# Optimization experiments

Hardware: AMD Instinct MI355X
Metric: run time of the kernel (lower is better)

The kernel has to match this reference:

```python
import jax, jax.numpy as jnp
import numpy as np

N_TX, N_ACC, N_MER = 100000, 50000, 5000
HID, HEADS, OUT_CH, LAYERS = 128, 4, 64, 3
HC = HID * HEADS  # 512, concat-heads width
SRC_T = ['tx', 'tx', 'tx', 'acc', 'acc', 'mer']
DST_T = ['acc', 'acc', 'mer', 'tx', 'tx', 'tx']


def setup_inputs():
    key = jax.random.key(0)
    ks = jax.random.split(key, 16)
    rn = lambda k, s: jax.random.normal(k, s, dtype=jnp.float32) * 0.05
    n_of = {'tx': N_TX, 'acc': N_ACC, 'mer': N_MER}
    E = N_TX  # one sender-acct / receiver-acct / merchant edge per transaction
    src = jnp.stack([jax.random.randint(jax.random.fold_in(ks[0], r), (E,), 0, n_of[SRC_T[r]]) for r in range(6)])
    dst = jnp.stack([jax.random.randint(jax.random.fold_in(ks[1], r), (E,), 0, n_of[DST_T[r]]) for r in range(6)])
    edges = jnp.stack([src, dst], axis=1).astype(jnp.int32)  # [6, 2, E] (rel, src/dst, edge)
    return dict(
        x_tx=rn(ks[2], (N_TX, 64)), x_acc=rn(ks[3], (N_ACC, 32)), x_mer=rn(ks[4], (N_MER, 32)),
        Wtx=rn(ks[5], (64, HID)), btx=jnp.zeros((HID,), jnp.float32),
        Wacc=rn(ks[6], (32, HID)), bacc=jnp.zeros((HID,), jnp.float32),
        Wmer=rn(ks[7], (32, HID)), bmer=jnp.zeros((HID,), jnp.float32),
        W0=rn(ks[8], (6, HID, HC)),            # layer-0 GAT linear per relation
        Wrest=rn(ks[9], (LAYERS - 1, 6, HC, HC)),  # layers 1..L-1
        att_s=rn(ks[10], (LAYERS, 6, HEADS, HID)),
        att_d=rn(ks[11], (LAYERS, 6, HEADS, HID)),
        att_b=jnp.zeros((LAYERS, 6, HC), jnp.float32),
        bn_g=jnp.ones((LAYERS, HC), jnp.float32), bn_b=jnp.zeros((LAYERS, HC), jnp.float32),
        Wh1=rn(ks[12], (HC, OUT_CH)), bh1=jnp.zeros((OUT_CH,), jnp.float32),
        Wh2=rn(ks[13], (OUT_CH, 1)), bh2=jnp.zeros((1,), jnp.float32),
        edges=edges)


def _gat_rel(x_src, x_dst, src, dst, W, a_s, a_d, b, n_dst):
    """PyG GATConv (shared lin, add_self_loops=False, concat heads), eval mode."""
    H, C = a_s.shape
    hs = (x_src @ W).reshape(-1, H, C)  # [Ns, H, C]
    hd = (x_dst @ W).reshape(-1, H, C)  # [Nd, H, C]
    e = jax.nn.leaky_relu((hs * a_s).sum(-1)[src] + (hd * a_d).sum(-1)[dst], 0.2)  # [E, H]
    m = jax.lax.stop_gradient(jax.ops.segment_max(e, dst, num_segments=n_dst))
    ex = jnp.exp(e - m[dst])
    denom = jax.ops.segment_sum(ex, dst, num_segments=n_dst)
    alpha = ex / (denom[dst] + 1e-16)  # segment softmax over in-edges of each dst
    out = jax.ops.segment_sum(alpha[:, :, None] * hs[src], dst, num_segments=n_dst)
    return out.reshape(n_dst, H * C) + b


def _forward(x_tx, x_acc, x_mer, Wtx, btx, Wacc, bacc, Wmer, bmer, W0, Wrest,
             att_s, att_d, att_b, bn_g, bn_b, Wh1, bh1, Wh2, bh2, edges):
    h = {'tx': jax.nn.relu(x_tx @ Wtx + btx),
         'acc': jax.nn.relu(x_acc @ Wacc + bacc),
         'mer': jax.nn.relu(x_mer @ Wmer + bmer)}
    n_of = {'tx': x_tx.shape[0], 'acc': x_acc.shape[0], 'mer': x_mer.shape[0]}
    for i in range(LAYERS):
        Wl = W0 if i == 0 else Wrest[i - 1]
        new = {k: jnp.zeros((n_of[k], HC), x_tx.dtype) for k in n_of}  # HeteroConv aggr='sum'
        for r in range(6):
            o = _gat_rel(h[SRC_T[r]], h[DST_T[r]], edges[r, 0], edges[r, 1],
                         Wl[r], att_s[i, r], att_d[i, r], att_b[i, r], n_of[DST_T[r]])
            new[DST_T[r]] = new[DST_T[r]] + o
        t = new['tx']  # BatchNorm1d (batch statistics) on transaction nodes only
        mu = t.mean(0)
        var = t.var(0)
        new['tx'] = (t - mu) / jnp.sqrt(var + 1e-5) * bn_g[i] + bn_b[i]
        new = {k: jax.nn.relu(v) for k, v in new.items()}
        if i > 0:  # residual from second layer on
            new = {k: new[k] + h[k] for k in new}
        h = new
    hidden = jax.nn.relu(h['tx'] @ Wh1 + bh1)
    return (hidden @ Wh2 + bh2).squeeze(-1)  # [N_tx] logits


def reference(x_tx, x_acc, x_mer, Wtx, btx, Wacc, bacc, Wmer, bmer, W0, Wrest,
              att_s, att_d, att_b, bn_g, bn_b, Wh1, bh1, Wh2, bh2, edges):
    return _forward(x_tx, x_acc, x_mer, Wtx, btx, Wacc, bacc, Wmer, bmer, W0, Wrest,
                    att_s, att_d, att_b, bn_g, bn_b, Wh1, bh1, Wh2, bh2, edges)
```

## Files before the change

kernel.cpp:

```cpp
#include <hip/hip_runtime.h>
#include <math.h>


typedef unsigned short BF16;
typedef short short8 __attribute__((ext_vector_type(8)));
typedef float f32x4 __attribute__((ext_vector_type(4)));
typedef __bf16 bf16x8 __attribute__((ext_vector_type(8)));

static __device__ __forceinline__ float lrelu(float x){ return x > 0.f ? x : 0.2f*x; }

__device__ __forceinline__ float ldE(const float* p, long i){ return p[i]; }
__device__ __forceinline__ float ldE(const BF16* p, long i){
  return __uint_as_float((unsigned)p[i] << 16);
}
__device__ __forceinline__ void stE(float* p, long i, float v){ p[i] = v; }
__device__ __forceinline__ void stE(BF16* p, long i, float v){
  unsigned u = __float_as_uint(v);
  p[i] = (BF16)((u + 0x7FFFu + ((u >> 16) & 1u)) >> 16);
}
__device__ __forceinline__ BF16 f2bf(float v){
  unsigned u = __float_as_uint(v);
  return (BF16)((u + 0x7FFFu + ((u >> 16) & 1u)) >> 16);
}
__device__ __forceinline__ float bf2f(short s){
  return __uint_as_float((unsigned)(unsigned short)s << 16);
}
__device__ __forceinline__ float4 ld4E(const float* p, long i){ return *(const float4*)(p + i); }
__device__ __forceinline__ float4 ld4E(const BF16* p, long i){
  ushort4 s = *(const ushort4*)(p + i);
  return make_float4(__uint_as_float((unsigned)s.x<<16), __uint_as_float((unsigned)s.y<<16),
                     __uint_as_float((unsigned)s.z<<16), __uint_as_float((unsigned)s.w<<16));
}

__global__ void k_zero(int* __restrict__ p, long n){
  long i = (long)blockIdx.x*blockDim.x + threadIdx.x;
  if (i < n) p[i] = 0;
}
__global__ void k_fill_f32(float* __restrict__ p, long n, float v){
  long i = (long)blockIdx.x*blockDim.x + threadIdx.x;
  if (i < n) p[i] = v;
}

__global__ __launch_bounds__(256) void k_wt(const float* __restrict__ in, BF16* __restrict__ out,
                                            int K, int N)
{
  in  += (long)blockIdx.z*K*N;
  out += (long)blockIdx.z*N*K;
  __shared__ float t[32][33];
  int kb = blockIdx.y*32, nb = blockIdx.x*32;
  int tx = threadIdx.x & 31, ty8 = threadIdx.x >> 5;
  for (int j = ty8; j < 32; j += 8){
    int k = kb + j, n = nb + tx;
    t[j][tx] = (k < K && n < N) ? in[(long)k*N + n] : 0.f;
  }
  __syncthreads();
  for (int j = ty8; j < 32; j += 8){
    int n = nb + j, k = kb + tx;
    if (n < N && k < K) out[(long)n*K + k] = f2bf(t[tx][j]);
  }
}

__global__ __launch_bounds__(256) void k_foldAll(
    const float* __restrict__ Wbase, long wstride,
    const float* __restrict__ atts, const float* __restrict__ attd,
    float* __restrict__ F, int Din)
{
  int w = (blockIdx.x*256 + threadIdx.x) >> 6;
  int lane = threadIdx.x & 63;
  int total = 48*Din;
  if (w >= total) return;
  int k = w % Din;
  int rem = w / Din;
  int h = rem & 3, sd = (rem >> 2) & 1, r = rem >> 3;
  const float* wr = Wbase + (long)r*wstride + (long)k*512 + h*128;
  const float* ar = (sd ? attd : atts) + r*512 + h*128;
  float p = wr[lane]*ar[lane] + wr[lane+64]*ar[lane+64];
  #pragma unroll
  for (int off = 32; off; off >>= 1) p += __shfl_down(p, off, 64);
  if (lane == 0) F[(long)((r*2+sd)*4 + h)*Din + k] = p;
}

template<int BN, int WM, int WN, int FM, int FN, typename TC>
__global__ __launch_bounds__(256) void k_mfma(
    const BF16* __restrict__ A, const BF16* __restrict__ Bt, TC* __restrict__ C,
    int M, int K, int c0, int ldc, int lda, const float* __restrict__ bias,
    int doRelu, int accum, long aZst, long cZst, int c0Zst, const BF16* __restrict__ Bt1)
{
  constexpr int BM = 128;
  constexpr int LSTR = 72;
  __shared__ __attribute__((aligned(16))) short Als[BM][LSTR];
  __shared__ __attribute__((aligned(16))) short Bls[BN][LSTR];
  const int z = blockIdx.z;
  A += (long)z*aZst;
  C += (long)z*cZst;
  c0 += z*c0Zst;
  if (z >= 1 && Bt1) Bt = Bt1;
  const int bn0 = blockIdx.x * BN;
  const int bm = blockIdx.y*BM;
  const int tid = threadIdx.x;
  const int wave = tid >> 6, lane = tid & 63;
  const int wr = wave / WN, wc = wave % WN;
  const int lrow = lane & 15, kg = lane >> 4;
  f32x4 acc[FM][FN] = {};
  for (int k0 = 0; k0 < K; k0 += 64){
    #pragma unroll
    for (int t = 0; t < 4; ++t){
      int idx = tid + t*256;
      int row = idx >> 3, kc = (idx & 7) << 3;
      int gr = bm + row;
      short8 v = {};
      if (gr < M) v = *(const short8*)(A + (long)gr*lda + k0 + kc);
      *(short8*)&Als[row][kc] = v;
    }
    #pragma unroll
    for (int t = 0; t < BN/32; ++t){
      int idx = tid + t*256;
      int row = idx >> 3, kc = (idx & 7) << 3;
      *(short8*)&Bls[row][kc] = *(const short8*)(Bt + (long)(c0+bn0+row)*K + k0 + kc);
    }
    __syncthreads();
    #pragma unroll
    for (int kk = 0; kk < 2; ++kk){
      short8 af[FM], bq[FN];
      #pragma unroll
      for (int m = 0; m < FM; ++m)
        af[m] = *(const short8*)&Als[wr*FM*16 + m*16 + lrow][kk*32 + kg*8];
      #pragma unroll
      for (int n = 0; n < FN; ++n)
        bq[n] = *(const short8*)&Bls[wc*FN*16 + n*16 + lrow][kk*32 + kg*8];
      #pragma unroll
      for (int m = 0; m < FM; ++m)
        #pragma unroll
        for (int n = 0; n < FN; ++n)
          acc[m][n] = __builtin_amdgcn_mfma_f32_16x16x32_bf16(
              __builtin_bit_cast(bf16x8, af[m]), __builtin_bit_cast(bf16x8, bq[n]),
              acc[m][n], 0, 0, 0);
    }
    __syncthreads();
  }
  #pragma unroll
  for (int m = 0; m < FM; ++m){
    #pragma unroll
    for (int n = 0; n < FN; ++n){
      #pragma unroll
      for (int j = 0; j < 4; ++j){
        int row = bm + wr*FM*16 + m*16 + kg*4 + j;
        if (row >= M) continue;
        int col = wc*FN*16 + n*16 + lrow;
        float v = acc[m][n][j];
        if (bias) v += bias[bn0 + col];
        if (doRelu) v = fmaxf(v, 0.f);
        long idx = (long)row*ldc + bn0 + col;
        if (accum) v += ldE(C, idx);
        stE(C, idx, v);
      }
    }
  }
}

template<typename TA, typename TC>
__global__ __launch_bounds__(256) void k_gemm(
    const TA* __restrict__ A, const float* __restrict__ B, TC* __restrict__ C,
    int M, int N, int K, int ldb, const float* __restrict__ bias, int doRelu)
{
  __shared__ float As[16][64];
  __shared__ float Bs[16][64];
  const int bm = blockIdx.y*64, bn = blockIdx.x*64;
  const int tid = threadIdx.x;
  const int ty = tid >> 4, tx = tid & 15;
  const int ar = tid >> 2;
  const int ac = (tid & 3) << 2;
  const int br = tid >> 4;
  const int bc = (tid & 15) << 2;
  float acc[4][4] = {};
  for (int k0 = 0; k0 < K; k0 += 16){
    int row = bm + ar;
    float4 av = make_float4(0.f,0.f,0.f,0.f);
    if (row < M) av = ld4E(A, (long)row*K + k0 + ac);
    As[ac+0][ar]=av.x; As[ac+1][ar]=av.y; As[ac+2][ar]=av.z; As[ac+3][ar]=av.w;
    float4 bv = make_float4(0.f,0.f,0.f,0.f);
    if (bn + bc + 3 < N) bv = *(const float4*)(B + (long)(k0+br)*ldb + bn + bc);
    *(float4*)&Bs[br][bc] = bv;
    __syncthreads();
    #pragma unroll
    for (int kk = 0; kk < 16; ++kk){
      float a[4], b[4];
      #pragma unroll
      for (int x = 0; x < 4; ++x){ a[x]=As[kk][ty*4+x]; b[x]=Bs[kk][tx*4+x]; }
      #pragma unroll
      for (int y = 0; y < 4; ++y)
        #pragma unroll
        for (int x = 0; x < 4; ++x) acc[y][x] += a[y]*b[x];
    }
    __syncthreads();
  }
  #pragma unroll
  for (int y = 0; y < 4; ++y){
    int row = bm + ty*4 + y;
    if (row >= M) continue;
    #pragma unroll
    for (int x = 0; x < 4; ++x){
      int col = bn + tx*4 + x;
      if (col >= N) continue;
      float v = acc[y][x];
      if (bias) v += bias[col];
      if (doRelu) v = fmaxf(v, 0.f);
      stE(C, (long)row*N + col, v);
    }
  }
}

template<int R>
__global__ __launch_bounds__(256) void k_scoreM(
    const BF16* __restrict__ X, const float* __restrict__ Ftab, long fstride,
    float* __restrict__ out, long ostride, int N, int Din)
{
  int wave = threadIdx.x >> 6, lane = threadIdx.x & 63;
  int node0 = blockIdx.x*16 + wave*4;
  if (node0 >= N) return;
  int base = lane*8;
  bool act = base < Din;
  float x[4][8];
  #pragma unroll
  for (int t = 0; t < 4; ++t){
    int node = node0 + t;
    if (act && node < N){
      short8 v = *(const short8*)(X + (long)node*Din + base);
      #pragma unroll
      for (int j = 0; j < 8; ++j) x[t][j] = bf2f(v[j]);
    } else {
      #pragma unroll
      for (int j = 0; j < 8; ++j) x[t][j] = 0.f;
    }
  }
  #pragma unroll
  for (int r = 0; r < R; ++r){
    const float* F = Ftab + (long)r*fstride;
    float p[4][4] = {};
    #pragma unroll
    for (int h = 0; h < 4; ++h){
      float f[8];
      if (act){
        float4 fa = *(const float4*)(F + h*Din + base);
        float4 fb = *(const float4*)(F + h*Din + base + 4);
        f[0]=fa.x; f[1]=fa.y; f[2]=fa.z; f[3]=fa.w;
        f[4]=fb.x; f[5]=fb.y; f[6]=fb.z; f[7]=fb.w;
      } else {
        #pragma unroll
        for (int j = 0; j < 8; ++j) f[j] = 0.f;
      }
      #pragma unroll
      for (int t = 0; t < 4; ++t)
        #pragma unroll
        for (int j = 0; j < 8; ++j) p[t][h] += x[t][j]*f[j];
    }
    #pragma unroll
    for (int t = 0; t < 4; ++t)
      #pragma unroll
      for (int h = 0; h < 4; ++h)
        #pragma unroll
        for (int off = 32; off; off >>= 1)
          p[t][h] += __shfl_down(p[t][h], off, 64);
    if (lane == 0){
      #pragma unroll
      for (int t = 0; t < 4; ++t){
        int node = node0 + t;
        if (node < N){
          #pragma unroll
          for (int h = 0; h < 4; ++h)
            out[(long)r*ostride + (long)node*4 + h] = p[t][h];
        }
      }
    }
  }
}

__global__ void k_hist(const int* __restrict__ dst, int* __restrict__ counts, int E, int nd){
  int e = blockIdx.x*blockDim.x + threadIdx.x;
  if (e >= E) return;
  int d = dst[e];
  if ((unsigned)d < (unsigned)nd) atomicAdd(&counts[d], 1);
}
__global__ void k_scan1(const int* __restrict__ counts, int* __restrict__ indptr,
                        int* __restrict__ bsums, int n)
{
  __shared__ int sm[256];
  int i = blockIdx.x*256 + threadIdx.x;
  int v = (i < n) ? counts[i] : 0;
  sm[threadIdx.x] = v; __syncthreads();
  for (int off = 1; off < 256; off <<= 1){
    int t = (threadIdx.x >= off) ? sm[threadIdx.x - off] : 0;
    __syncthreads();
    sm[threadIdx.x] += t;
    __syncthreads();
  }
  if (i < n) indptr[i+1] = sm[threadIdx.x];
  if (threadIdx.x == 255) bsums[blockIdx.x] = sm[255];
  if (blockIdx.x == 0 && threadIdx.x == 0) indptr[0] = 0;
}
__global__ void k_scan2(int* __restrict__ bsums, int nb){
  __shared__ int sm[1024];
  int t = threadIdx.x;
  int v = (t < nb) ? bsums[t] : 0;
  sm[t] = v; __syncthreads();
  for (int off = 1; off < 1024; off <<= 1){
    int x = (t >= off) ? sm[t - off] : 0;
    __syncthreads();
    sm[t] += x;
    __syncthreads();
  }
  if (t < nb) bsums[t] = sm[t];
}
__global__ void k_scan3(int* __restrict__ indptr, const int* __restrict__ bsums, int n){
  if (blockIdx.x == 0) return;
  int i = blockIdx.x*256 + threadIdx.x;
  int add = bsums[blockIdx.x - 1];
  if (i < n) indptr[i+1] += add;
}
__global__ void k_scatter(const int* __restrict__ src, const int* __restrict__ dst,
                          const int* __restrict__ indptr, int* __restrict__ cursor,
                          int* __restrict__ esrc, int E, int nd, int ns)
{
  int e = blockIdx.x*blockDim.x + threadIdx.x;
  if (e >= E) return;
  int d = dst[e];
  if ((unsigned)d >= (unsigned)nd) return;
  int s = src[e];
  if ((unsigned)s >= (unsigned)ns) s = 0;
  int pos = indptr[d] + atomicAdd(&cursor[d], 1);
  if (pos >= 0 && pos < E) esrc[pos] = s;
}

struct AlphaArgs {
  const float* ss[3]; const float* sd[3];
  const int* ip[3]; const int* es[3];
  float* al[3]; int nd[3]; int ns[3];
};
__global__ __launch_bounds__(256) void k_alpha3b(AlphaArgs a, int E){
  int r = blockIdx.y;
  int wid = (blockIdx.x*blockDim.x + threadIdx.x) >> 6;
  int lane = threadIdx.x & 63;
  if (wid >= a.nd[r]) return;
  const int* indptr = a.ip[r];
  const int* esrc = a.es[r];
  const float* ss = a.ss[r];
  int ns = a.ns[r];
  int e0 = indptr[wid], e1 = indptr[wid+1];
  e0 = max(0, min(e0, E)); e1 = max(e0, min(e1, E));
  if (e0 >= e1) return;
  int h = lane >> 4, g = lane & 15;
  float sdl = a.sd[r][(long)wid*4 + h];
  float* alpha = a.al[r];
  float m = -INFINITY;
  for (int e = e0 + g; e < e1; e += 16){
    int s = esrc[e]; if ((unsigned)s >= (unsigned)ns) s = 0;
    m = fmaxf(m, lrelu(ss[(long)s*4 + h] + sdl));
  }
  #pragma unroll
  for (int o = 1; o < 16; o <<= 1) m = fmaxf(m, __shfl_xor(m, o, 16));
  float den = 0.f;
  for (int e = e0 + g; e < e1; e += 16){
    int s = esrc[e]; if ((unsigned)s >= (unsigned)ns) s = 0;
    den += __expf(lrelu(ss[(long)s*4 + h] + sdl) - m);
  }
  #pragma unroll
  for (int o = 1; o < 16; o <<= 1) den += __shfl_xor(den, o, 16);
  float inv = 1.f/(den + 1e-16f);
  for (int e = e0 + g; e < e1; e += 16){
    int s = esrc[e]; if ((unsigned)s >= (unsigned)ns) s = 0;
    alpha[(long)e*4 + h] = __expf(lrelu(ss[(long)s*4 + h] + sdl) - m) * inv;
  }
}

template<int NJ>
__global__ __launch_bounds__(256) void k_gather4(
    const BF16* __restrict__ A, const float* __restrict__ alpha,
    const int* __restrict__ indptr, const int* __restrict__ esrc,
    BF16* __restrict__ G, int n_dst, int Din, int E, int ns)
{
  int wid = (blockIdx.x*blockDim.x + threadIdx.x) >> 6;
  int lane = threadIdx.x & 63;
  if (wid >= n_dst) return;
  int e0 = indptr[wid], e1 = indptr[wid+1];
  e0 = max(0, min(e0, E)); e1 = max(e0, min(e1, E));
  float acc[4][NJ];
  #pragma unroll
  for (int h = 0; h < 4; ++h)
    #pragma unroll
    for (int j = 0; j < NJ; ++j) acc[h][j] = 0.f;
  for (int e = e0; e < e1; ++e){
    int s = esrc[e]; if ((unsigned)s >= (unsigned)ns) s = 0;
    float a0 = alpha[(long)e*4 + 0], a1 = alpha[(long)e*4 + 1];
    float a2 = alpha[(long)e*4 + 2], a3 = alpha[(long)e*4 + 3];
    const BF16* ar = A + (long)s*Din;
    if (NJ == 8){
      short8 v = *(const short8*)(ar + lane*8);
      #pragma unroll
      for (int j = 0; j < NJ; ++j){
        float x = bf2f(v[j]);
        acc[0][j] += a0*x; acc[1][j] += a1*x; acc[2][j] += a2*x; acc[3][j] += a3*x;
      }
    } else {
      ushort2 v = *(const ushort2*)(ar + lane*2);
      float x0 = bf2f((short)v.x), x1 = bf2f((short)v.y);
      acc[0][0] += a0*x0; acc[1][0] += a1*x0; acc[2][0] += a2*x0; acc[3][0] += a3*x0;
      acc[0][1] += a0*x1; acc[1][1] += a1*x1; acc[2][1] += a2*x1; acc[3][1] += a3*x1;
    }
  }
  #pragma unroll
  for (int h = 0; h < 4; ++h){
    if (NJ == 8){
      short8 g;
      #pragma unroll
      for (int j = 0; j < NJ; ++j) g[j] = (short)f2bf(acc[h][j]);
      *(short8*)(G + ((long)wid*4 + h)*Din + lane*8) = g;
    } else {
      ushort2 g;
      g.x = f2bf(acc[h][0]); g.y = f2bf(acc[h][1]);
      *(ushort2*)(G + ((long)wid*4 + h)*Din + lane*2) = g;
    }
  }
}

template<int NJ>
__device__ __forceinline__ void agg_body(
    const BF16* __restrict__ Zt, const float* __restrict__ alpha,
    const int* __restrict__ indptr, const int* __restrict__ esrc,
    float* acc, int wid, int lane, int TW, int head0, int E, int ns)
{
  int e0 = indptr[wid], e1 = indptr[wid+1];
  e0 = max(0, min(e0, E)); e1 = max(e0, min(e1, E));
  for (int e = e0; e < e1; ++e){
    int s = esrc[e]; if ((unsigned)s >= (unsigned)ns) s = 0;
    float aA = alpha[(long)e*4 + head0];
    const BF16* zr = Zt + (long)s*TW;
    if (NJ == 2){
      ushort2 z = *(const ushort2*)(zr + lane*2);
      acc[0] += aA * bf2f((short)z.x);
      acc[1] += aA * bf2f((short)z.y);
    } else {
      acc[0] += aA * ldE(zr, lane);
    }
  }
}

template<int NJ>
__global__ __launch_bounds__(256) void k_agg2(
    const BF16* __restrict__ Z0, const BF16* __restrict__ Z1,
    const float* __restrict__ a0, const float* __restrict__ a1,
    const int* __restrict__ ip0, const int* __restrict__ ip1,
    const int* __restrict__ es0, const int* __restrict__ es1,
    BF16* __restrict__ out, int ldc, int c0w, int TW, int head0,
    int n_dst, int E, int ns0, int ns1)
{
  int wid = (blockIdx.x*blockDim.x + threadIdx.x) >> 6;
  int lane = threadIdx.x & 63;
  if (wid >= n_dst) return;
  float acc[NJ];
  #pragma unroll
  for (int j = 0; j < NJ; ++j) acc[j] = 0.f;
  agg_body<NJ>(Z0, a0, ip0, es0, acc, wid, lane, TW, head0, E, ns0);
  agg_body<NJ>(Z1, a1, ip1, es1, acc, wid, lane, TW, head0, E, ns1);
  if (NJ == 2){
    ushort2 g; g.x = f2bf(acc[0]); g.y = f2bf(acc[1]);
    *(ushort2*)(out + (long)wid*ldc + c0w + lane*2) = g;
  } else {
    stE(out, (long)wid*ldc + c0w + lane, acc[0]);
  }
}

template<int NJ>
__global__ __launch_bounds__(256) void k_agg3(
    const BF16* __restrict__ Z0, const BF16* __restrict__ Z1, const BF16* __restrict__ Z2,
    const float* __restrict__ a0, const float* __restrict__ a1, const float* __restrict__ a2,
    const int* __restrict__ ip0, const int* __restrict__ ip1, const int* __restrict__ ip2,
    const int* __restrict__ es0, const int* __restrict__ es1, const int* __restrict__ es2,
    BF16* __restrict__ out, int ldc, int TW, int head0,
    int n_dst, int E, int ns0, int ns1, int ns2)
{
  int wid = (blockIdx.x*blockDim.x + threadIdx.x) >> 6;
  int lane = threadIdx.x & 63;
  if (wid >= n_dst) return;
  float acc[NJ];
  #pragma unroll
  for (int j = 0; j < NJ; ++j) acc[j] = 0.f;
  agg_body<NJ>(Z0, a0, ip0, es0, acc, wid, lane, TW, head0, E, ns0);
  agg_body<NJ>(Z1, a1, ip1, es1, acc, wid, lane, TW, head0, E, ns1);
  agg_body<NJ>(Z2, a2, ip2, es2, acc, wid, lane, TW, head0, E, ns2);
  if (NJ == 2){
    ushort2 g; g.x = f2bf(acc[0]); g.y = f2bf(acc[1]);
    *(ushort2*)(out + (long)wid*ldc + lane*2) = g;
  } else {
    stE(out, (long)wid*ldc + lane, acc[0]);
  }
}

__global__ void k_bnp(const BF16* __restrict__ nw, float* __restrict__ bnp,
                      int N, int TW, int P)
{
  int col  = threadIdx.x & (TW - 1);
  int slot = threadIdx.x / TW;
  int rpb  = 256 / TW;
  int p    = blockIdx.x*rpb + slot;
  float s = 0.f, s2 = 0.f;
  for (long r = p; r < N; r += P){
    float v = ldE(nw, r*TW + col);
    s += v; s2 += v*v;
  }
  bnp[(long)p*2*TW + col]      = s;
  bnp[(long)p*2*TW + TW + col] = s2;
}
__global__ void k_bnf(const float* __restrict__ bnp, float* __restrict__ bns,
                      int P, int TW)
{
  int c = blockIdx.x*256 + threadIdx.x;
  if (c >= 2*TW) return;
  float s = 0.f;
  for (int p = 0; p < P; ++p) s += bnp[(long)p*2*TW + c];
  bns[c] = s;
}
__global__ void k_bn_apply(const BF16* __restrict__ nw, const float* __restrict__ bns,
                           const float* __restrict__ g, const float* __restrict__ b,
                           BF16* __restrict__ A, int N, int TW, int c0, int res)
{
  long total8 = (long)N*TW/8;
  for (long i8 = (long)blockIdx.x*blockDim.x + threadIdx.x; i8 < total8;
       i8 += (long)gridDim.x*blockDim.x){
    long i = i8*8;
    int col = (int)(i % TW);
    long r  = i / TW;
    short8 nv = *(const short8*)(nw + i);
    long ai = r*512 + c0 + col;
    short8 av;
    if (res) av = *(const short8*)(A + ai);
    short8 ov;
    #pragma unroll
    for (int k = 0; k < 8; ++k){
      int gc = c0 + col + k;
      float mu  = bns[col+k] / (float)N;
      float var = bns[TW + col + k] / (float)N - mu*mu;
      float sc = g[gc] * rsqrtf(var + 1e-5f);
      float sh = b[gc] - mu*sc;
      float v = fmaxf(bf2f(nv[k])*sc + sh, 0.f);
      if (res) v += bf2f(av[k]);
      ov[k] = (short)f2bf(v);
    }
    *(short8*)(A + ai) = ov;
  }
}

__global__ void k_update(const BF16* __restrict__ B, const float* __restrict__ ab1,
                         const float* __restrict__ ab2, BF16* __restrict__ A,
                         long n512, int res)
{
  long n8 = n512/8;
  for (long i8 = (long)blockIdx.x*blockDim.x + threadIdx.x; i8 < n8;
       i8 += (long)gridDim.x*blockDim.x){
    long i = i8*8;
    int c = (int)(i & 511);
    short8 bv = *(const short8*)(B + i);
    short8 av;
    if (res) av = *(const short8*)(A + i);
    short8 ov;
    #pragma unroll
    for (int k = 0; k < 8; ++k){
      float v = bf2f(bv[k]) + ab1[c+k] + (ab2 ? ab2[c+k] : 0.f);
      v = fmaxf(v, 0.f);
      if (res) v += bf2f(av[k]);
      ov[k] = (short)f2bf(v);
    }
    *(short8*)(A + i) = ov;
  }
}

__global__ void k_logits(const BF16* __restrict__ Hid, const float* __restrict__ Wh2,
                         const float* __restrict__ bh2, float* __restrict__ out, int N)
{
  int node = (blockIdx.x*blockDim.x + threadIdx.x) >> 6;
  int lane = threadIdx.x & 63;
  if (node >= N) return;
  float v = ldE(Hid, (long)node*64 + lane) * Wh2[lane];
  #pragma unroll
  for (int off = 32; off; off >>= 1) v += __shfl_down(v, off, 64);
  if (lane == 0) out[node] = v + bh2[0];
}

struct Arena {
  BF16 *A[3];
  BF16 *Bst[3];
  BF16 *Zt;
  BF16 *blkB;
  BF16 *hidden;
  float *scoreS, *scoreD;
  float *alpha;
  float *Fbuf;
  float *bnp, *bns;
  int *counts, *bsums;
  int *indptr[6], *esrc[6];
  BF16 *Wt0[6], *WtL[2][6], *Wh1t;
  size_t total;
};

extern "C" void kernel_launch(void* const* d_in, const int* in_sizes, int n_in,
                              void* d_out, int out_size, void* d_ws, size_t ws_size,
                              hipStream_t stream)
{
  const float* x_tx  = (const float*)d_in[0];
  const float* x_acc = (const float*)d_in[1];
  const float* x_mer = (const float*)d_in[2];
  const float* Wtx = (const float*)d_in[3];  const float* btx  = (const float*)d_in[4];
  const float* Wacc= (const float*)d_in[5];  const float* bacc = (const float*)d_in[6];
  const float* Wmer= (const float*)d_in[7];  const float* bmer = (const float*)d_in[8];
  const float* W0   = (const float*)d_in[9];
  const float* Wrest= (const float*)d_in[10];
  const float* att_s= (const float*)d_in[11];
  const float* att_d= (const float*)d_in[12];
  const float* att_b= (const float*)d_in[13];
  const float* bn_g = (const float*)d_in[14];
  const float* bn_b = (const float*)d_in[15];
  const float* Wh1  = (const float*)d_in[16]; const float* bh1 = (const float*)d_in[17];
  const float* Wh2  = (const float*)d_in[18]; const float* bh2 = (const float*)d_in[19];
  const int*   edges= (const int*)d_in[20];

  const int E    = in_sizes[20] / 12;
  const int nTx  = in_sizes[0] / 64;
  const int nAcc = in_sizes[1] / 32;
  const int nMer = in_sizes[2] / 32;
  const int nOf[3]   = {nTx, nAcc, nMer};
  const int SRC_T[6] = {0,0,0,1,1,2};
  const int DST_T[6] = {1,1,2,0,0,0};
  const int maxN = max(nTx, max(nAcc, nMer));
  (void)n_in;

  auto layout = [&](int TW)->Arena{
    Arena P{};
    size_t off = 0;
    auto a = [&](size_t bytes)->char*{
      char* p = (char*)d_ws + off;
      off += (bytes + 255) & ~(size_t)255;
      return p;
    };
    auto al = [](size_t b){ return (b + 255) & ~(size_t)255; };
    P.A[0]   = (BF16*)a((size_t)nTx *512*2);
    P.A[1]   = (BF16*)a((size_t)nAcc*512*2);
    P.A[2]   = (BF16*)a((size_t)nMer*512*2);
    P.Bst[1] = (BF16*)a((size_t)nAcc*512*2);
    P.Bst[2] = (BF16*)a((size_t)nMer*512*2);
    size_t zrowsA = (size_t)maxN > (size_t)2*nAcc + nMer ? (size_t)maxN : (size_t)2*nAcc + nMer;
    size_t blkA = al(zrowsA*TW*2);
    size_t blkBsz = al((size_t)nTx*TW*2);
    size_t gB = al((size_t)nMer*4*512*2);
    if (gB > blkBsz) blkBsz = gB;
    size_t scoreB = al((size_t)3*maxN*4*4)*2;
    size_t hidB = al((size_t)nTx*64*2);
    size_t scr = blkA + blkBsz;
    if (scr < scoreB) scr = scoreB;
    if (scr < hidB)   scr = hidB;
    char* scrBase = a(scr);
    P.Zt     = (BF16*)scrBase;
    P.blkB   = (BF16*)(scrBase + blkA);
    P.scoreS = (float*)scrBase;
    P.scoreD = (float*)(scrBase + al((size_t)3*maxN*4*4));
    P.hidden = (BF16*)scrBase;
    P.alpha  = (float*)a((size_t)3*E*4*4);
    P.Fbuf   = (float*)a((size_t)6*8*512*4);
    P.bnp    = (float*)a(262144);
    P.bns    = (float*)a(4096);
    P.counts = (int*)a((size_t)maxN*4);
    P.bsums  = (int*)a(4096);
    for (int r = 0; r < 6; ++r){
      P.indptr[r] = (int*)a((size_t)(nOf[DST_T[r]]+1)*4);
      P.esrc[r]   = (int*)a((size_t)E*4);
    }
    for (int r = 0; r < 6; ++r) P.Wt0[r] = (BF16*)a((size_t)512*128*2);
    for (int l = 0; l < 2; ++l)
      for (int r = 0; r < 6; ++r) P.WtL[l][r] = (BF16*)a((size_t)512*512*2);
    P.Wh1t = (BF16*)a((size_t)64*512*2);
    P.total = off;
    return P;
  };

  int TW = 0;
  Arena P{};
  for (int cand : {128, 64}){
    P = layout(cand);
    if (P.total <= ws_size){ TW = cand; break; }
  }
  if (TW == 0){
    float sentinel = 10000.0f + (float)(ws_size >> 20);
    k_fill_f32<<<dim3((out_size+255)/256), dim3(256), 0, stream>>>((float*)d_out, (long)out_size, sentinel);
    return;
  }
  const int nTiles = 512 / TW;
  const int NJv = TW/64;
  const int rpb = 256 / TW, PBX = 64, Pp = PBX * rpb;
  dim3 b256(256);

  k_wt<<<dim3(16,4,6),  b256, 0, stream>>>(W0,    P.Wt0[0],    128, 512);
  k_wt<<<dim3(16,16,12),b256, 0, stream>>>(Wrest, P.WtL[0][0], 512, 512);
  k_wt<<<dim3(2,16,1),  b256, 0, stream>>>(Wh1,   P.Wh1t,      512, 64);

  auto mfma_gemm = [&](const BF16* A, const BF16* Bt, BF16* Cp, int M, int K, int c0, int ldc){
    if (TW >= 128)
      k_mfma<128,2,2,4,4,BF16><<<dim3(TW/128,(M+127)/128,1),b256,0,stream>>>(
          A, Bt, Cp, M, K, c0, ldc, K, (const float*)nullptr, 0, 0, 0L, 0L, 0, (const BF16*)nullptr);
    else
      k_mfma<64,4,1,2,4,BF16><<<dim3(1,(M+127)/128,1),b256,0,stream>>>(
          A, Bt, Cp, M, K, c0, ldc, K, (const float*)nullptr, 0, 0, 0L, 0L, 0, (const BF16*)nullptr);
  };
  auto mfma_pair = [&](const BF16* A, const BF16* Bt0, const BF16* Bt1p, BF16* Cp, long cZst,
                       int M, int K, int c0){
    if (TW >= 128)
      k_mfma<128,2,2,4,4,BF16><<<dim3(TW/128,(M+127)/128,2),b256,0,stream>>>(
          A, Bt0, Cp, M, K, c0, TW, K, (const float*)nullptr, 0, 0, 0L, cZst, 0, Bt1p);
    else {
      mfma_gemm(A, Bt0, Cp, M, K, c0, TW);
      mfma_gemm(A, Bt1p, Cp + cZst, M, K, c0, TW);
    }
  };

  for (int r = 0; r < 6; ++r){
    int nd = nOf[DST_T[r]], ns = nOf[SRC_T[r]];
    const int* srcP = edges + (size_t)r*2*E;
    const int* dstP = srcP + E;
    int nb = (nd + 255)/256;
    k_zero   <<<dim3(nb),          b256, 0, stream>>>(P.counts, (long)nd);
    k_hist   <<<dim3((E+255)/256), b256, 0, stream>>>(dstP, P.counts, E, nd);
    k_scan1  <<<dim3(nb),          b256, 0, stream>>>(P.counts, P.indptr[r], P.bsums, nd);
    k_scan2  <<<dim3(1),           dim3(1024),0, stream>>>(P.bsums, nb);
    k_scan3  <<<dim3(nb),          b256, 0, stream>>>(P.indptr[r], P.bsums, nd);
    k_zero   <<<dim3(nb),          b256, 0, stream>>>(P.counts, (long)nd);
    k_scatter<<<dim3((E+255)/256), b256, 0, stream>>>(srcP, dstP, P.indptr[r], P.counts, P.esrc[r], E, nd, ns);
  }

  k_gemm<float,BF16><<<dim3(2,(nTx +63)/64), b256, 0, stream>>>(x_tx,  Wtx,  P.A[0], nTx,  128, 64, 128, btx,  1);
  k_gemm<float,BF16><<<dim3(2,(nAcc+63)/64), b256, 0, stream>>>(x_acc, Wacc, P.A[1], nAcc, 128, 32, 128, bacc, 1);
  k_gemm<float,BF16><<<dim3(2,(nMer+63)/64), b256, 0, stream>>>(x_mer, Wmer, P.A[2], nMer, 128, 32, 128, bmer, 1);

  const long mS = (long)maxN*4;
  for (int i = 0; i < 3; ++i){
    const int Din = (i == 0) ? 128 : 512;
    const int res = (i > 0) ? 1 : 0;
    const long fstr = 8L*Din;
    const float* WbaseL = (i == 0) ? W0 : (Wrest + (size_t)(i-1)*6*512*512);
    const long wstride = (i == 0) ? 128L*512 : 512L*512;
    auto Wtof = [&](int r)->const BF16*{ return (i == 0) ? P.Wt0[r] : P.WtL[i-1][r]; };

    k_foldAll<<<dim3(48*Din/4), b256, 0, stream>>>(WbaseL, wstride,
        att_s + (size_t)i*6*512, att_d + (size_t)i*6*512, P.Fbuf, Din);

    k_scoreM<3><<<dim3((nTx+15)/16), b256, 0, stream>>>(P.A[0], P.Fbuf,           fstr, P.scoreS, mS, nTx, Din);
    k_scoreM<2><<<dim3((nAcc+15)/16), b256, 0, stream>>>(P.A[1], P.Fbuf + 4*Din,  fstr, P.scoreD, mS, nAcc, Din);
    k_scoreM<1><<<dim3((nMer+15)/16), b256, 0, stream>>>(P.A[2], P.Fbuf + 20*Din, fstr, P.scoreD + 2*mS, 0, nMer, Din);
    {
      AlphaArgs aa{};
      int ndMax = 0;
      for (int r = 0; r < 3; ++r){
        aa.ss[r] = P.scoreS + r*mS; aa.sd[r] = P.scoreD + r*mS;
        aa.ip[r] = P.indptr[r]; aa.es[r] = P.esrc[r];
        aa.al[r] = P.alpha + (size_t)r*E*4;
        aa.nd[r] = nOf[DST_T[r]]; aa.ns[r] = nTx;
        if (aa.nd[r] > ndMax) ndMax = aa.nd[r];
      }
      k_alpha3b<<<dim3((ndMax+3)/4,3), b256, 0, stream>>>(aa, E);
    }
    {
      BF16* Gm = P.blkB;
      if (Din == 512)
        k_gather4<8><<<dim3((nMer+3)/4), b256, 0, stream>>>(P.A[0], P.alpha + (size_t)2*E*4,
            P.indptr[2], P.esrc[2], Gm, nMer, Din, E, nTx);
      else
        k_gather4<2><<<dim3((nMer+3)/4), b256, 0, stream>>>(P.A[0], P.alpha + (size_t)2*E*4,
            P.indptr[2], P.esrc[2], Gm, nMer, Din, E, nTx);
      k_mfma<128,2,2,4,4,BF16><<<dim3(1,(nMer+127)/128,4), b256, 0, stream>>>(
          Gm, Wtof(2), P.Bst[2], nMer, Din, 0, 512, 4*Din,
          (const float*)nullptr, 0, 0, (long)Din, 128L, 128, (const BF16*)nullptr);
    }
    {
      BF16* Zr0 = P.Zt;
      BF16* Zr1 = P.blkB;
      long zst = (long)(Zr1 - Zr0);
      for (int t = 0; t < nTiles; ++t){
        int c0 = t*TW;
        mfma_pair(P.A[0], Wtof(0), Wtof(1), Zr0, zst, nTx, Din, c0);
        dim3 ga((nAcc+3)/4);
        if (NJv == 2)
          k_agg2<2><<<ga,b256,0,stream>>>(Zr0, Zr1, P.alpha, P.alpha + (size_t)E*4,
              P.indptr[0], P.indptr[1], P.esrc[0], P.esrc[1],
              P.Bst[1], 512, c0, TW, c0>>7, nAcc, E, nTx, nTx);
        else
          k_agg2<1><<<ga,b256,0,stream>>>(Zr0, Zr1, P.alpha, P.alpha + (size_t)E*4,
              P.indptr[0], P.indptr[1], P.esrc[0], P.esrc[1],
              P.Bst[1], 512, c0, TW, c0>>7, nAcc, E, nTx, nTx);
      }
    }

    k_scoreM<2><<<dim3((nAcc+15)/16), b256, 0, stream>>>(P.A[1], P.Fbuf + 24*Din, fstr, P.scoreS, mS, nAcc, Din);
    k_scoreM<1><<<dim3((nMer+15)/16), b256, 0, stream>>>(P.A[2], P.Fbuf + 40*Din, fstr, P.scoreS + 2*mS, 0, nMer, Din);
    k_scoreM<3><<<dim3((nTx+15)/16), b256, 0, stream>>>(P.A[0], P.Fbuf + 28*Din, fstr, P.scoreD, mS, nTx, Din);
    {
      AlphaArgs aa{};
      for (int q = 0; q < 3; ++q){
        int r = 3 + q;
        aa.ss[q] = P.scoreS + q*mS; aa.sd[q] = P.scoreD + q*mS;
        aa.ip[q] = P.indptr[r]; aa.es[q] = P.esrc[r];
        aa.al[q] = P.alpha + (size_t)q*E*4;
        aa.nd[q] = nTx; aa.ns[q] = nOf[SRC_T[r]];
      }
      k_alpha3b<<<dim3((nTx+3)/4,3), b256, 0, stream>>>(aa, E);
    }
    BF16* Z3 = P.Zt;
    BF16* Z4 = P.Zt + (size_t)nAcc*TW;
    BF16* Z5 = P.Zt + (size_t)2*nAcc*TW;
    BF16* nw = P.blkB;
    for (int t = 0; t < nTiles; ++t){
      int c0 = t*TW;
      mfma_pair(P.A[1], Wtof(3), Wtof(4), Z3, (long)nAcc*TW, nAcc, Din, c0);
      mfma_gemm(P.A[2], Wtof(5), Z5, nMer, Din, c0, TW);
      dim3 ga((nTx+3)/4);
      if (NJv == 2)
        k_agg3<2><<<ga,b256,0,stream>>>(Z3,Z4,Z5, P.alpha, P.alpha+(size_t)E*4, P.alpha+(size_t)2*E*4,
            P.indptr[3],P.indptr[4],P.indptr[5], P.esrc[3],P.esrc[4],P.esrc[5],
            nw, TW, TW, c0>>7, nTx, E, nAcc, nAcc, nMer);
      else
        k_agg3<1><<<ga,b256,0,stream>>>(Z3,Z4,Z5, P.alpha, P.alpha+(size_t)E*4, P.alpha+(size_t)2*E*4,
            P.indptr[3],P.indptr[4],P.indptr[5], P.esrc[3],P.esrc[4],P.esrc[5],
            nw, TW, TW, c0>>7, nTx, E, nAcc, nAcc, nMer);
      k_bnp<<<dim3(PBX), b256, 0, stream>>>(nw, P.bnp, nTx, TW, Pp);
      k_bnf<<<dim3((2*TW+255)/256), b256, 0, stream>>>(P.bnp, P.bns, Pp, TW);
      k_bn_apply<<<dim3(2048), b256, 0, stream>>>(nw, P.bns,
          bn_g + (size_t)i*512, bn_b + (size_t)i*512, P.A[0], nTx, TW, c0, res);
    }
    const float* ab0 = att_b + ((size_t)(i*6 + 0))*512;
    const float* ab1 = att_b + ((size_t)(i*6 + 1))*512;
    const float* ab2 = att_b + ((size_t)(i*6 + 2))*512;
    k_update<<<dim3(1024), b256, 0, stream>>>(P.Bst[1], ab0, ab1, P.A[1], (long)nAcc*512, res);
    k_update<<<dim3(128),  b256, 0, stream>>>(P.Bst[2], ab2, (const float*)nullptr, P.A[2], (long)nMer*512, res);
  }

  k_mfma<64,4,1,2,4,BF16><<<dim3(1,(nTx+127)/128,1), b256, 0, stream>>>(
      P.A[0], P.Wh1t, P.hidden, nTx, 512, 0, 64, 512, bh1, 1, 0,
      0L, 0L, 0, (const BF16*)nullptr);
  k_logits<<<dim3((nTx+3)/4), b256, 0, stream>>>(P.hidden, Wh2, bh2, (float*)d_out, nTx);
}
```

Before: 10.12 ms.

## Load GEMM tiles directly to LDS and vectorize BatchNorm partial sums

The MFMA GEMM now stages A and B tiles with global_load_lds (direct global-to-LDS DMA) instead of loading into registers and storing to LDS. The LDS layout drops its padding to the dense 64-wide rows that this instruction requires, and out-of-range rows are clamped to a valid row rather than zero-filled. The BatchNorm partial-sum kernel reads 8 bf16 values per thread with more partial slots, which needs a larger partial buffer. Removing the padding may bring LDS bank conflicts back on the fragment reads.

```diff
diff --git a/kernel.cpp b/kernel.cpp
--- a/kernel.cpp
+++ b/kernel.cpp
@@ -30,6 +30,12 @@
   ushort4 s = *(const ushort4*)(p + i);
   return make_float4(__uint_as_float((unsigned)s.x<<16), __uint_as_float((unsigned)s.y<<16),
                      __uint_as_float((unsigned)s.z<<16), __uint_as_float((unsigned)s.w<<16));
+}
+
+__device__ __forceinline__ void gl_lds16(const BF16* g, short* l){
+  __builtin_amdgcn_global_load_lds(
+      (const __attribute__((address_space(1))) void*)g,
+      (__attribute__((address_space(3))) void*)l, 16, 0, 0);
 }
 
 __global__ void k_zero(int* __restrict__ p, long n){
@@ -87,9 +93,8 @@
     int doRelu, int accum, long aZst, long cZst, int c0Zst, const BF16* __restrict__ Bt1)
 {
   constexpr int BM = 128;
-  constexpr int LSTR = 72;
-  __shared__ __attribute__((aligned(16))) short Als[BM][LSTR];
-  __shared__ __attribute__((aligned(16))) short Bls[BN][LSTR];
+  __shared__ __attribute__((aligned(16))) short AlsL[BM*64];
+  __shared__ __attribute__((aligned(16))) short BlsL[BN*64];
   const int z = blockIdx.z;
   A += (long)z*aZst;
   C += (long)z*cZst;
@@ -101,22 +106,22 @@
   const int wave = tid >> 6, lane = tid & 63;
   const int wr = wave / WN, wc = wave % WN;
   const int lrow = lane & 15, kg = lane >> 4;
+  const int lr8 = lane >> 3, lc8 = (lane & 7) << 3;
   f32x4 acc[FM][FN] = {};
   for (int k0 = 0; k0 < K; k0 += 64){
     #pragma unroll
-    for (int t = 0; t < 4; ++t){
-      int idx = tid + t*256;
-      int row = idx >> 3, kc = (idx & 7) << 3;
+    for (int t = 0; t < BM/32; ++t){
+      int rb = (wave*(BM/32) + t)*8;
+      int row = rb + lr8;
       int gr = bm + row;
-      short8 v = {};
-      if (gr < M) v = *(const short8*)(A + (long)gr*lda + k0 + kc);
-      *(short8*)&Als[row][kc] = v;
+      if (gr >= M) gr = bm;
+      gl_lds16(A + (long)gr*lda + k0 + lc8, &AlsL[rb*64]);
     }
     #pragma unroll
     for (int t = 0; t < BN/32; ++t){
-      int idx = tid + t*256;
-      int row = idx >> 3, kc = (idx & 7) << 3;
-      *(short8*)&Bls[row][kc] = *(const short8*)(Bt + (long)(c0+bn0+row)*K + k0 + kc);
+      int rb = (wave*(BN/32) + t)*8;
+      int row = rb + lr8;
+      gl_lds16(Bt + (long)(c0+bn0+row)*K + k0 + lc8, &BlsL[rb*64]);
     }
     __syncthreads();
     #pragma unroll
@@ -124,10 +129,10 @@
       short8 af[FM], bq[FN];
       #pragma unroll
       for (int m = 0; m < FM; ++m)
-        af[m] = *(const short8*)&Als[wr*FM*16 + m*16 + lrow][kk*32 + kg*8];
+        af[m] = *(const short8*)&AlsL[(wr*FM*16 + m*16 + lrow)*64 + kk*32 + kg*8];
       #pragma unroll
       for (int n = 0; n < FN; ++n)
-        bq[n] = *(const short8*)&Bls[wc*FN*16 + n*16 + lrow][kk*32 + kg*8];
+        bq[n] = *(const short8*)&BlsL[(wc*FN*16 + n*16 + lrow)*64 + kk*32 + kg*8];
       #pragma unroll
       for (int m = 0; m < FM; ++m)
         #pragma unroll
@@ -498,17 +503,25 @@
 __global__ void k_bnp(const BF16* __restrict__ nw, float* __restrict__ bnp,
                       int N, int TW, int P)
 {
-  int col  = threadIdx.x & (TW - 1);
-  int slot = threadIdx.x / TW;
-  int rpb  = 256 / TW;
+  int cpr  = TW/8;
+  int col  = (threadIdx.x % cpr)*8;
+  int slot = threadIdx.x / cpr;
+  int rpb  = 256 / cpr;
   int p    = blockIdx.x*rpb + slot;
-  float s = 0.f, s2 = 0.f;
+  float s[8] = {}, s2[8] = {};
   for (long r = p; r < N; r += P){
-    float v = ldE(nw, r*TW + col);
-    s += v; s2 += v*v;
-  }
-  bnp[(long)p*2*TW + col]      = s;
-  bnp[(long)p*2*TW + TW + col] = s2;
+    short8 v = *(const short8*)(nw + r*TW + col);
+    #pragma unroll
+    for (int k = 0; k < 8; ++k){
+      float x = bf2f(v[k]);
+      s[k] += x; s2[k] += x*x;
+    }
+  }
+  #pragma unroll
+  for (int k = 0; k < 8; ++k){
+    bnp[(long)p*2*TW + col + k]      = s[k];
+    bnp[(long)p*2*TW + TW + col + k] = s2[k];
+  }
 }
 __global__ void k_bnf(const float* __restrict__ bnp, float* __restrict__ bns,
                       int P, int TW)
@@ -664,7 +677,7 @@
     P.hidden = (BF16*)scrBase;
     P.alpha  = (float*)a((size_t)3*E*4*4);
     P.Fbuf   = (float*)a((size_t)6*8*512*4);
-    P.bnp    = (float*)a(262144);
+    P.bnp    = (float*)a(1048576);
     P.bns    = (float*)a(4096);
     P.counts = (int*)a((size_t)maxN*4);
     P.bsums  = (int*)a(4096);
@@ -693,7 +706,7 @@
   }
   const int nTiles = 512 / TW;
   const int NJv = TW/64;
-  const int rpb = 256 / TW, PBX = 64, Pp = PBX * rpb;
+  const int PBX = 64, Pp = PBX * (256/(TW/8));
   dim3 b256(256);
 
   k_wt<<<dim3(16,4,6),  b256, 0, stream>>>(W0,    P.Wt0[0],    128, 512);
```

Result: slower. 17.81 ms (+76.1%).

## Fuse paired relation GEMMs into one 128x256 MFMA kernel sharing A tiles

Applied to the files above, without the earlier changes.

Adds a 512-thread MFMA kernel, k_mfma2, that computes both projections of the paired GEMM in a single block. It stages one A tile in LDS and a combined 256-row B tile built from Bt0 and Bt1, then writes the two 128-column halves to separate outputs. Before, a z=2 grid launched two blocks per row tile, and each loaded the same A tile. The change is meant to halve A global traffic and cut the block count, at the cost of more LDS per block, a larger accumulator footprint and possibly lower occupancy. The new launch uses a grid x-dimension of 1, so it assumes a tile width of 128.

```diff
diff --git a/kernel.cpp b/kernel.cpp
--- a/kernel.cpp
+++ b/kernel.cpp
@@ -153,6 +153,75 @@
         long idx = (long)row*ldc + bn0 + col;
         if (accum) v += ldE(C, idx);
         stE(C, idx, v);
+      }
+    }
+  }
+}
+
+__global__ __launch_bounds__(512) void k_mfma2(
+    const BF16* __restrict__ A, const BF16* __restrict__ Bt0, const BF16* __restrict__ Bt1,
+    BF16* __restrict__ C0, BF16* __restrict__ C1,
+    int M, int K, int c0, int ldc, int lda)
+{
+  constexpr int BM = 128, BN = 256, LSTR = 72;
+  __shared__ __attribute__((aligned(16))) short Als[BM][LSTR];
+  __shared__ __attribute__((aligned(16))) short Bls[BN][LSTR];
+  const int bm = blockIdx.y*BM;
+  const int tid = threadIdx.x;
+  const int wave = tid >> 6, lane = tid & 63;
+  const int wr = wave >> 2, wc = wave & 3;
+  const int lrow = lane & 15, kg = lane >> 4;
+  f32x4 acc[4][4] = {};
+  for (int k0 = 0; k0 < K; k0 += 64){
+    #pragma unroll
+    for (int t = 0; t < 2; ++t){
+      int idx = tid + t*512;
+      int row = idx >> 3, kc = (idx & 7) << 3;
+      int gr = bm + row;
+      short8 v = {};
+      if (gr < M) v = *(const short8*)(A + (long)gr*lda + k0 + kc);
+      *(short8*)&Als[row][kc] = v;
+    }
+    #pragma unroll
+    for (int t = 0; t < 4; ++t){
+      int idx = tid + t*512;
+      int row = idx >> 3, kc = (idx & 7) << 3;
+      const BF16* src = (row < 128) ? (Bt0 + (long)(c0 + row)*K)
+                                    : (Bt1 + (long)(c0 + row - 128)*K);
+      *(short8*)&Bls[row][kc] = *(const short8*)(src + k0 + kc);
+    }
+    __syncthreads();
+    #pragma unroll
+    for (int kk = 0; kk < 2; ++kk){
+      short8 af[4], bq[4];
+      #pragma unroll
+      for (int m = 0; m < 4; ++m)
+        af[m] = *(const short8*)&Als[wr*64 + m*16 + lrow][kk*32 + kg*8];
+      #pragma unroll
+      for (int n = 0; n < 4; ++n)
+        bq[n] = *(const short8*)&Bls[wc*64 + n*16 + lrow][kk*32 + kg*8];
+      #pragma unroll
+      for (int m = 0; m < 4; ++m)
+        #pragma unroll
+        for (int n = 0; n < 4; ++n)
+          acc[m][n] = __builtin_amdgcn_mfma_f32_16x16x32_bf16(
+              __builtin_bit_cast(bf16x8, af[m]), __builtin_bit_cast(bf16x8, bq[n]),
+              acc[m][n], 0, 0, 0);
+    }
+    __syncthreads();
+  }
+  #pragma unroll
+  for (int m = 0; m < 4; ++m){
+    #pragma unroll
+    for (int n = 0; n < 4; ++n){
+      #pragma unroll
+      for (int j = 0; j < 4; ++j){
+        int row = bm + wr*64 + m*16 + kg*4 + j;
+        if (row >= M) continue;
+        int col = wc*64 + n*16 + lrow;
+        BF16* C = (col < 128) ? C0 : C1;
+        int cc = (col < 128) ? col : col - 128;
+        stE(C, (long)row*ldc + cc, acc[m][n][j]);
       }
     }
   }
@@ -711,8 +780,8 @@
   auto mfma_pair = [&](const BF16* A, const BF16* Bt0, const BF16* Bt1p, BF16* Cp, long cZst,
                        int M, int K, int c0){
     if (TW >= 128)
-      k_mfma<128,2,2,4,4,BF16><<<dim3(TW/128,(M+127)/128,2),b256,0,stream>>>(
-          A, Bt0, Cp, M, K, c0, TW, K, (const float*)nullptr, 0, 0, 0L, cZst, 0, Bt1p);
+      k_mfma2<<<dim3(1,(M+127)/128,1), dim3(512), 0, stream>>>(
+          A, Bt0, Bt1p, Cp, Cp + cZst, M, K, c0, TW, K);
     else {
       mfma_gemm(A, Bt0, Cp, M, K, c0, TW);
       mfma_gemm(A, Bt1p, Cp + cZst, M, K, c0, TW);
```

Measured after the change: 10.14 ms (median of 2 runs). No clear change (+0.2%).
